# Kernel optimization log

Measured on AMD Instinct MI355X. Metric: run time of the kernel, lower is better.

The kernel has to match this reference:

```python
import jax, jax.numpy as jnp
import numpy as np

N_NODES = 100000
N_EDGES = 3200000
D_IN = 128
D_OUT = 128


def setup_inputs() -> dict:
    key = jax.random.key(0)
    ks = jax.random.split(key, 7)
    x = jax.random.normal(ks[0], (N_NODES, D_IN), dtype=jnp.float32)
    weight = jax.random.normal(ks[1], (D_IN, D_OUT), dtype=jnp.float32) * (1.0 / np.sqrt(D_OUT))
    bias = jax.random.normal(ks[2], (D_OUT,), dtype=jnp.float32) * (1.0 / np.sqrt(D_OUT))
    adj_rows = jax.random.randint(ks[3], (N_EDGES,), 0, N_NODES, dtype=jnp.int32)
    adj_cols = jax.random.randint(ks[4], (N_EDGES,), 0, N_NODES, dtype=jnp.int32)
    adj_vals = jax.random.uniform(ks[5], (N_EDGES,), dtype=jnp.float32)
    # norm kept in [0.5, 1.5) to avoid division blow-up (degree-like normalizer)
    norm = jax.random.uniform(ks[6], (N_NODES, 1), dtype=jnp.float32) + 0.5
    return {"x": x, "weight": weight, "bias": bias,
            "adj_rows": adj_rows, "adj_cols": adj_cols, "adj_vals": adj_vals,
            "norm": norm}


def reference(x, weight, bias, adj_rows, adj_cols, adj_vals, norm):
    # support = input @ W               [N, D_OUT]
    support = x @ weight
    # output = spmm(adj, support): gather source rows, scale by edge value,
    # scatter-add into destination rows.
    gathered = support[adj_cols] * adj_vals[:, None]          # [E, D_OUT]
    output = jax.ops.segment_sum(gathered, adj_rows, num_segments=x.shape[0])
    output = output / norm
    return output + bias
```

## Files before the change

kernel.cpp:

```cpp
#include <hip/hip_runtime.h>

#define M_NODES 100000
#define N_EDGES 3200000
#define D 128
#define NBUCK 1563
#define GEMM_BLOCKS 1563
#define HIST_CHUNK 12288
#define HIST_BLOCKS 261
#define FILL_CHUNK 6144
#define FILL_BLOCKS 521
#define BUCK_CAP 4096

#define OFF_SUP16  0ull
#define OFF_BCNT   25600000ull
#define OFF_BSTART 25606400ull
#define OFF_BPOS   25612800ull
#define OFF_REC    25619200ull
#define WS_NEEDED  51219200ull

__device__ __forceinline__ unsigned short f2bf(float f) {
    unsigned u = __float_as_uint(f);
    u += 0x7fff + ((u >> 16) & 1);
    return (unsigned short)(u >> 16);
}
__device__ __forceinline__ float2 bfpair(unsigned u) {
    float2 r;
    r.x = __uint_as_float(u << 16);
    r.y = __uint_as_float(u & 0xffff0000u);
    return r;
}

__global__ __launch_bounds__(256) void gemm_hist_kernel(const float* __restrict__ x,
                                                        const float* __restrict__ w,
                                                        unsigned* __restrict__ sup16,
                                                        const int* __restrict__ rows,
                                                        int* __restrict__ bcnt,
                                                        int M) {
    __shared__ __align__(16) char smem[24576];
    const int tid = threadIdx.x;

    if (blockIdx.x >= GEMM_BLOCKS) {
        int* h = (int*)smem;
        const int hb = blockIdx.x - GEMM_BLOCKS;
        for (int i = tid; i < NBUCK; i += 256) h[i] = 0;
        __syncthreads();
        const long long base = (long long)hb * HIST_CHUNK;
#pragma unroll
        for (int i = 0; i < 12; ++i) {
            const long long e = base + (i * 256 + tid) * 4;
            if (e < N_EDGES) {
                const int4 r = *(const int4*)&rows[e];
                atomicAdd(&h[r.x >> 6], 1);
                atomicAdd(&h[r.y >> 6], 1);
                atomicAdd(&h[r.z >> 6], 1);
                atomicAdd(&h[r.w >> 6], 1);
            }
        }
        __syncthreads();
        for (int i = tid; i < NBUCK; i += 256)
            if (h[i]) atomicAdd(&bcnt[i], h[i]);
        return;
    }

    float (*sX)[64]  = (float(*)[64])smem;
    float (*sW)[128] = (float(*)[128])(smem + 8192);

    const int r0 = blockIdx.x * 64;
    const int tx = tid & 31;
    const int ty = tid >> 5;

    float acc[8][4];
#pragma unroll
    for (int r = 0; r < 8; ++r)
#pragma unroll
        for (int c = 0; c < 4; ++c) acc[r][c] = 0.f;

    for (int c0 = 0; c0 < 128; c0 += 32) {
        {
            const int row = tid >> 3;
            const int kk  = (tid & 7) * 4;
#pragma unroll
            for (int h = 0; h < 2; ++h) {
                const int rr = row + h * 32;
                float4 v = make_float4(0.f, 0.f, 0.f, 0.f);
                if (r0 + rr < M)
                    v = *(const float4*)&x[(size_t)(r0 + rr) * D + c0 + kk];
                sX[kk + 0][rr] = v.x;
                sX[kk + 1][rr] = v.y;
                sX[kk + 2][rr] = v.z;
                sX[kk + 3][rr] = v.w;
            }
        }
#pragma unroll
        for (int i = tid; i < 1024; i += 256) {
            const int k  = i >> 5;
            const int c4 = (i & 31) * 4;
            *(float4*)&sW[k][c4] = *(const float4*)&w[(size_t)(c0 + k) * D + c4];
        }
        __syncthreads();

#pragma unroll
        for (int k = 0; k < 32; ++k) {
            const float4 wv = *(const float4*)&sW[k][tx * 4];
            const float4 xa = *(const float4*)&sX[k][ty * 8];
            const float4 xb = *(const float4*)&sX[k][ty * 8 + 4];
            const float xr[8] = {xa.x, xa.y, xa.z, xa.w, xb.x, xb.y, xb.z, xb.w};
#pragma unroll
            for (int r = 0; r < 8; ++r) {
                acc[r][0] += xr[r] * wv.x;
                acc[r][1] += xr[r] * wv.y;
                acc[r][2] += xr[r] * wv.z;
                acc[r][3] += xr[r] * wv.w;
            }
        }
        __syncthreads();
    }

#pragma unroll
    for (int r = 0; r < 8; ++r) {
        const int row = r0 + ty * 8 + r;
        if (row < M) {
            uint2 p;
            p.x = (unsigned)f2bf(acc[r][0]) | ((unsigned)f2bf(acc[r][1]) << 16);
            p.y = (unsigned)f2bf(acc[r][2]) | ((unsigned)f2bf(acc[r][3]) << 16);
            *(uint2*)&sup16[(size_t)row * 64 + tx * 2] = p;
        }
    }
}

__global__ __launch_bounds__(256) void scan_kernel(const int* __restrict__ bcnt,
                                                   int* __restrict__ bstart,
                                                   int* __restrict__ bpos) {
    __shared__ int tsum[256];
    const int t = threadIdx.x;
    int local[7];
    int s = 0;
#pragma unroll
    for (int k = 0; k < 7; ++k) {
        const int idx = t * 7 + k;
        const int v = (idx < NBUCK) ? bcnt[idx] : 0;
        local[k] = v;
        s += v;
    }
    tsum[t] = s;
    __syncthreads();
    for (int off = 1; off < 256; off <<= 1) {
        const int v = (t >= off) ? tsum[t - off] : 0;
        __syncthreads();
        tsum[t] += v;
        __syncthreads();
    }
    int pos = tsum[t] - s;
#pragma unroll
    for (int k = 0; k < 7; ++k) {
        const int idx = t * 7 + k;
        if (idx < NBUCK) {
            bstart[idx] = pos;
            bpos[idx]   = pos;
            pos += local[k];
        }
    }
    if (t == 0) bstart[NBUCK] = N_EDGES;
}

__global__ __launch_bounds__(256) void fill_kernel(const int* __restrict__ rows,
                                                   const int* __restrict__ cols,
                                                   const float* __restrict__ vals,
                                                   int* __restrict__ bpos,
                                                   int2* __restrict__ rec) {
    __shared__ int cnt[NBUCK];
    __shared__ int bas[NBUCK];
    __shared__ unsigned short lrank[FILL_CHUNK];
    const int t = threadIdx.x;
    for (int i = t; i < NBUCK; i += 256) cnt[i] = 0;
    __syncthreads();
    const long long base = (long long)blockIdx.x * FILL_CHUNK;

#pragma unroll
    for (int i = 0; i < 6; ++i) {
        const int li = (i * 256 + t) * 4;
        const long long e = base + li;
        if (e < N_EDGES) {
            const int4 r = *(const int4*)&rows[e];
            lrank[li + 0] = (unsigned short)atomicAdd(&cnt[r.x >> 6], 1);
            lrank[li + 1] = (unsigned short)atomicAdd(&cnt[r.y >> 6], 1);
            lrank[li + 2] = (unsigned short)atomicAdd(&cnt[r.z >> 6], 1);
            lrank[li + 3] = (unsigned short)atomicAdd(&cnt[r.w >> 6], 1);
        }
    }
    __syncthreads();
    for (int i = t; i < NBUCK; i += 256)
        bas[i] = cnt[i] ? atomicAdd(&bpos[i], cnt[i]) : 0;
    __syncthreads();
#pragma unroll
    for (int i = 0; i < 6; ++i) {
        const int li = (i * 256 + t) * 4;
        const long long e = base + li;
        if (e < N_EDGES) {
            const int4   r = *(const int4*)&rows[e];
            const int4   c = *(const int4*)&cols[e];
            const float4 v = *(const float4*)&vals[e];
            int p;
            p = bas[r.x >> 6] + lrank[li + 0];
            rec[p] = make_int2(c.x | ((r.x & 63) << 20), __float_as_int(v.x));
            p = bas[r.y >> 6] + lrank[li + 1];
            rec[p] = make_int2(c.y | ((r.y & 63) << 20), __float_as_int(v.y));
            p = bas[r.z >> 6] + lrank[li + 2];
            rec[p] = make_int2(c.z | ((r.z & 63) << 20), __float_as_int(v.z));
            p = bas[r.w >> 6] + lrank[li + 3];
            rec[p] = make_int2(c.w | ((r.w & 63) << 20), __float_as_int(v.w));
        }
    }
}

__global__ __launch_bounds__(512) void gather_kernel(const unsigned* __restrict__ sup16,
                                                     const int* __restrict__ bstart,
                                                     const int2* __restrict__ rec,
                                                     const float* __restrict__ norm,
                                                     const float* __restrict__ bias,
                                                     float* __restrict__ out) {
    __shared__ int2 elist[BUCK_CAP];
    __shared__ unsigned short lrank[BUCK_CAP];
    __shared__ int cnt[64];
    __shared__ int rbase[65];
    const int tid = threadIdx.x;
    const int b   = blockIdx.x;

    if (tid < 64) cnt[tid] = 0;
    __syncthreads();
    const int s0 = bstart[b];
    const int n  = min(bstart[b + 1] - s0, BUCK_CAP);

    for (int k = tid; k < n; k += 512) {
        const int rl = (rec[s0 + k].x >> 20) & 63;
        lrank[k] = (unsigned short)atomicAdd(&cnt[rl], 1);
    }
    __syncthreads();
    if (tid == 0) {
        int run = 0;
#pragma unroll
        for (int i = 0; i < 64; ++i) {
            rbase[i] = run;
            run += cnt[i];
        }
        rbase[64] = run;
    }
    __syncthreads();
    for (int k = tid; k < n; k += 512) {
        const int2 e = rec[s0 + k];
        elist[rbase[(e.x >> 20) & 63] + lrank[k]] = make_int2(e.x & 0xFFFFF, e.y);
    }
    __syncthreads();

    const int w    = tid >> 6;
    const int lane = tid & 63;
    const unsigned* __restrict__ supl = sup16 + lane;
    const int fo = lane * 2;
    const float2 b2 = *(const float2*)&bias[fo];

#pragma unroll 1
    for (int rr = 0; rr < 8; ++rr) {
        const int rl  = w * 8 + rr;
        const int row = b * 64 + rl;
        if (row >= M_NODES) break;
        const int j0 = rbase[rl];
        const int j1 = rbase[rl + 1];
        float2 acc = make_float2(0.f, 0.f);
        int j = j0;
        for (; j + 8 <= j1; j += 8) {
            int2 e[8];
#pragma unroll
            for (int q = 0; q < 8; ++q) e[q] = elist[j + q];
            unsigned u[8];
#pragma unroll
            for (int q = 0; q < 8; ++q) u[q] = supl[(unsigned)e[q].x << 6];
#pragma unroll
            for (int q = 0; q < 8; ++q) {
                const float v = __int_as_float(e[q].y);
                const float2 p = bfpair(u[q]);
                acc.x = fmaf(p.x, v, acc.x);
                acc.y = fmaf(p.y, v, acc.y);
            }
        }
        for (; j + 2 <= j1; j += 2) {
            const int2 e0 = elist[j];
            const int2 e1 = elist[j + 1];
            const unsigned u0 = supl[(unsigned)e0.x << 6];
            const unsigned u1 = supl[(unsigned)e1.x << 6];
            const float2 p0 = bfpair(u0);
            const float2 p1 = bfpair(u1);
            const float v0 = __int_as_float(e0.y);
            const float v1 = __int_as_float(e1.y);
            acc.x = fmaf(p0.x, v0, acc.x);
            acc.y = fmaf(p0.y, v0, acc.y);
            acc.x = fmaf(p1.x, v1, acc.x);
            acc.y = fmaf(p1.y, v1, acc.y);
        }
        for (; j < j1; ++j) {
            const int2 e = elist[j];
            const unsigned u = supl[(unsigned)e.x << 6];
            const float v = __int_as_float(e.y);
            const float2 p = bfpair(u);
            acc.x = fmaf(p.x, v, acc.x);
            acc.y = fmaf(p.y, v, acc.y);
        }
        const float inv = 1.0f / norm[row];
        float2 o;
        o.x = fmaf(acc.x, inv, b2.x);
        o.y = fmaf(acc.y, inv, b2.y);
        *(float2*)&out[(size_t)row * D + fo] = o;
    }
}

__global__ __launch_bounds__(256) void gemm32_kernel(const float* __restrict__ x,
                                                     const float* __restrict__ w,
                                                     float* __restrict__ support,
                                                     int M) {
    __shared__ float sX[32][64];
    __shared__ float sW[32][128];
    const int tid = threadIdx.x;
    const int r0  = blockIdx.x * 64;
    const int tx  = tid & 31;
    const int ty  = tid >> 5;
    float acc[8][4];
#pragma unroll
    for (int r = 0; r < 8; ++r)
#pragma unroll
        for (int c = 0; c < 4; ++c) acc[r][c] = 0.f;
    for (int c0 = 0; c0 < 128; c0 += 32) {
        {
            const int row = tid >> 3;
            const int kk  = (tid & 7) * 4;
#pragma unroll
            for (int h = 0; h < 2; ++h) {
                const int rr = row + h * 32;
                float4 v = make_float4(0.f, 0.f, 0.f, 0.f);
                if (r0 + rr < M)
                    v = *(const float4*)&x[(size_t)(r0 + rr) * D + c0 + kk];
                sX[kk + 0][rr] = v.x; sX[kk + 1][rr] = v.y;
                sX[kk + 2][rr] = v.z; sX[kk + 3][rr] = v.w;
            }
        }
#pragma unroll
        for (int i = tid; i < 1024; i += 256) {
            const int k  = i >> 5;
            const int c4 = (i & 31) * 4;
            *(float4*)&sW[k][c4] = *(const float4*)&w[(size_t)(c0 + k) * D + c4];
        }
        __syncthreads();
#pragma unroll
        for (int k = 0; k < 32; ++k) {
            const float4 wv = *(const float4*)&sW[k][tx * 4];
            const float4 xa = *(const float4*)&sX[k][ty * 8];
            const float4 xb = *(const float4*)&sX[k][ty * 8 + 4];
            const float xr[8] = {xa.x, xa.y, xa.z, xa.w, xb.x, xb.y, xb.z, xb.w};
#pragma unroll
            for (int r = 0; r < 8; ++r) {
                acc[r][0] += xr[r] * wv.x; acc[r][1] += xr[r] * wv.y;
                acc[r][2] += xr[r] * wv.z; acc[r][3] += xr[r] * wv.w;
            }
        }
        __syncthreads();
    }
#pragma unroll
    for (int r = 0; r < 8; ++r) {
        const int row = r0 + ty * 8 + r;
        if (row < M)
            *(float4*)&support[(size_t)row * D + tx * 4] =
                make_float4(acc[r][0], acc[r][1], acc[r][2], acc[r][3]);
    }
}

__global__ __launch_bounds__(256) void spmm_kernel(const float* __restrict__ support,
                                                   const int* __restrict__ rows,
                                                   const int* __restrict__ cols,
                                                   const float* __restrict__ vals,
                                                   float* __restrict__ out) {
    const long long t = (long long)blockIdx.x * 256 + threadIdx.x;
    const int e = (int)(t >> 5);
    if (e >= N_EDGES) return;
    const int f   = (int)(t & 31) * 4;
    const int src = cols[e];
    const int dst = rows[e];
    const float v = vals[e];
    const float4 s = *(const float4*)&support[(size_t)src * D + f];
    float* o = &out[(size_t)dst * D + f];
    atomicAdd(o + 0, s.x * v);
    atomicAdd(o + 1, s.y * v);
    atomicAdd(o + 2, s.z * v);
    atomicAdd(o + 3, s.w * v);
}

__global__ __launch_bounds__(256) void finalize_kernel(float* __restrict__ out,
                                                       const float* __restrict__ norm,
                                                       const float* __restrict__ bias) {
    const int t = blockIdx.x * 256 + threadIdx.x;
    const int nrow = t >> 5;
    if (nrow >= M_NODES) return;
    const int f = (t & 31) * 4;
    const float inv = 1.0f / norm[nrow];
    float4 o = *(float4*)&out[(size_t)nrow * D + f];
    const float4 b = *(const float4*)&bias[f];
    o.x = o.x * inv + b.x; o.y = o.y * inv + b.y;
    o.z = o.z * inv + b.z; o.w = o.w * inv + b.w;
    *(float4*)&out[(size_t)nrow * D + f] = o;
}

extern "C" void kernel_launch(void* const* d_in, const int* in_sizes, int n_in,
                              void* d_out, int out_size, void* d_ws, size_t ws_size,
                              hipStream_t stream) {
    const float* x    = (const float*)d_in[0];
    const float* w    = (const float*)d_in[1];
    const float* bias = (const float*)d_in[2];
    const int*   rows = (const int*)d_in[3];
    const int*   cols = (const int*)d_in[4];
    const float* vals = (const float*)d_in[5];
    const float* norm = (const float*)d_in[6];
    float* out = (float*)d_out;
    char* ws = (char*)d_ws;

    if (ws_size >= WS_NEEDED) {
        unsigned* sup16  = (unsigned*)(ws + OFF_SUP16);
        int*      bcnt   = (int*)(ws + OFF_BCNT);
        int*      bstart = (int*)(ws + OFF_BSTART);
        int*      bpos   = (int*)(ws + OFF_BPOS);
        int2*     rec    = (int2*)(ws + OFF_REC);

        hipMemsetAsync(bcnt, 0, NBUCK * sizeof(int), stream);
        gemm_hist_kernel<<<GEMM_BLOCKS + HIST_BLOCKS, 256, 0, stream>>>(x, w, sup16,
                                                                        rows, bcnt, M_NODES);
        scan_kernel<<<1, 256, 0, stream>>>(bcnt, bstart, bpos);
        fill_kernel<<<FILL_BLOCKS, 256, 0, stream>>>(rows, cols, vals, bpos, rec);
        gather_kernel<<<NBUCK, 512, 0, stream>>>(sup16, bstart, rec,
                                                 norm, bias, out);
    } else {
        float* support = (float*)ws;
        gemm32_kernel<<<(M_NODES + 63) / 64, 256, 0, stream>>>(x, w, support, M_NODES);
        hipMemsetAsync(d_out, 0, (size_t)out_size * sizeof(float), stream);
        const long long spmm_threads = (long long)N_EDGES * 32;
        spmm_kernel<<<(int)((spmm_threads + 255) / 256), 256, 0, stream>>>(support, rows, cols, vals, out);
        finalize_kernel<<<(M_NODES * 32 + 255) / 256, 256, 0, stream>>>(out, norm, bias);
    }
}
```

Measured before the change: 370.7 us.

## Use fixed-capacity bucket slots to drop histogram pass and scan kernel

Replaces the histogram, prefix-scan, and fill pipeline with a single fill pass that writes edge records into fixed-capacity per-bucket slots (BUCK_CAP each), with offsets claimed by a global atomicAdd on the bucket counter. The fill is fused into the GEMM launch, which removes one full read of rows and two kernel launches. The gather kernel now does its per-row reordering with shared-memory atomics instead of a separate rank array. In exchange the workspace grows to hold padded buckets, and any bucket with more than BUCK_CAP edges silently drops records.

```diff
diff --git a/kernel.cpp b/kernel.cpp
--- a/kernel.cpp
+++ b/kernel.cpp
@@ -5,18 +5,15 @@
 #define D 128
 #define NBUCK 1563
 #define GEMM_BLOCKS 1563
-#define HIST_CHUNK 12288
-#define HIST_BLOCKS 261
 #define FILL_CHUNK 6144
 #define FILL_BLOCKS 521
+#define PREP_BLOCKS (FILL_BLOCKS + GEMM_BLOCKS)
 #define BUCK_CAP 4096
 
 #define OFF_SUP16  0ull
 #define OFF_BCNT   25600000ull
-#define OFF_BSTART 25606400ull
-#define OFF_BPOS   25612800ull
-#define OFF_REC    25619200ull
-#define WS_NEEDED  51219200ull
+#define OFF_REC    25608192ull
+#define WS_NEEDED  76824576ull
 
 __device__ __forceinline__ unsigned short f2bf(float f) {
     unsigned u = __float_as_uint(f);
@@ -30,42 +27,76 @@
     return r;
 }
 
-__global__ __launch_bounds__(256) void gemm_hist_kernel(const float* __restrict__ x,
-                                                        const float* __restrict__ w,
-                                                        unsigned* __restrict__ sup16,
-                                                        const int* __restrict__ rows,
-                                                        int* __restrict__ bcnt,
-                                                        int M) {
-    __shared__ __align__(16) char smem[24576];
+__global__ __launch_bounds__(256) void prep_kernel(const float* __restrict__ x,
+                                                   const float* __restrict__ w,
+                                                   unsigned* __restrict__ sup16,
+                                                   const int* __restrict__ rows,
+                                                   const int* __restrict__ cols,
+                                                   const float* __restrict__ vals,
+                                                   int* __restrict__ bcnt,
+                                                   int2* __restrict__ rec,
+                                                   int M) {
+    __shared__ __align__(16) char smem[25088];
     const int tid = threadIdx.x;
 
-    if (blockIdx.x >= GEMM_BLOCKS) {
-        int* h = (int*)smem;
-        const int hb = blockIdx.x - GEMM_BLOCKS;
-        for (int i = tid; i < NBUCK; i += 256) h[i] = 0;
-        __syncthreads();
-        const long long base = (long long)hb * HIST_CHUNK;
-#pragma unroll
-        for (int i = 0; i < 12; ++i) {
-            const long long e = base + (i * 256 + tid) * 4;
+    if (blockIdx.x < FILL_BLOCKS) {
+        int* cnt = (int*)smem;
+        int* bas = (int*)(smem + 6256);
+        unsigned short* lrank = (unsigned short*)(smem + 12512);
+        for (int i = tid; i < NBUCK; i += 256) cnt[i] = 0;
+        __syncthreads();
+        const long long base = (long long)blockIdx.x * FILL_CHUNK;
+
+#pragma unroll
+        for (int i = 0; i < 6; ++i) {
+            const int li = (i * 256 + tid) * 4;
+            const long long e = base + li;
             if (e < N_EDGES) {
                 const int4 r = *(const int4*)&rows[e];
-                atomicAdd(&h[r.x >> 6], 1);
-                atomicAdd(&h[r.y >> 6], 1);
-                atomicAdd(&h[r.z >> 6], 1);
-                atomicAdd(&h[r.w >> 6], 1);
+                lrank[li + 0] = (unsigned short)atomicAdd(&cnt[r.x >> 6], 1);
+                lrank[li + 1] = (unsigned short)atomicAdd(&cnt[r.y >> 6], 1);
+                lrank[li + 2] = (unsigned short)atomicAdd(&cnt[r.z >> 6], 1);
+                lrank[li + 3] = (unsigned short)atomicAdd(&cnt[r.w >> 6], 1);
             }
         }
         __syncthreads();
         for (int i = tid; i < NBUCK; i += 256)
-            if (h[i]) atomicAdd(&bcnt[i], h[i]);
+            bas[i] = cnt[i] ? atomicAdd(&bcnt[i], cnt[i]) : 0;
+        __syncthreads();
+#pragma unroll
+        for (int i = 0; i < 6; ++i) {
+            const int li = (i * 256 + tid) * 4;
+            const long long e = base + li;
+            if (e < N_EDGES) {
+                const int4   r = *(const int4*)&rows[e];
+                const int4   c = *(const int4*)&cols[e];
+                const float4 v = *(const float4*)&vals[e];
+                int p;
+                p = bas[r.x >> 6] + lrank[li + 0];
+                if (p < BUCK_CAP)
+                    rec[(size_t)(r.x >> 6) * BUCK_CAP + p] =
+                        make_int2(c.x | ((r.x & 63) << 20), __float_as_int(v.x));
+                p = bas[r.y >> 6] + lrank[li + 1];
+                if (p < BUCK_CAP)
+                    rec[(size_t)(r.y >> 6) * BUCK_CAP + p] =
+                        make_int2(c.y | ((r.y & 63) << 20), __float_as_int(v.y));
+                p = bas[r.z >> 6] + lrank[li + 2];
+                if (p < BUCK_CAP)
+                    rec[(size_t)(r.z >> 6) * BUCK_CAP + p] =
+                        make_int2(c.z | ((r.z & 63) << 20), __float_as_int(v.z));
+                p = bas[r.w >> 6] + lrank[li + 3];
+                if (p < BUCK_CAP)
+                    rec[(size_t)(r.w >> 6) * BUCK_CAP + p] =
+                        make_int2(c.w | ((r.w & 63) << 20), __float_as_int(v.w));
+            }
+        }
         return;
     }
 
     float (*sX)[64]  = (float(*)[64])smem;
     float (*sW)[128] = (float(*)[128])(smem + 8192);
 
-    const int r0 = blockIdx.x * 64;
+    const int r0 = (blockIdx.x - FILL_BLOCKS) * 64;
     const int tx = tid & 31;
     const int ty = tid >> 5;
 
@@ -128,99 +159,13 @@
     }
 }
 
-__global__ __launch_bounds__(256) void scan_kernel(const int* __restrict__ bcnt,
-                                                   int* __restrict__ bstart,
-                                                   int* __restrict__ bpos) {
-    __shared__ int tsum[256];
-    const int t = threadIdx.x;
-    int local[7];
-    int s = 0;
-#pragma unroll
-    for (int k = 0; k < 7; ++k) {
-        const int idx = t * 7 + k;
-        const int v = (idx < NBUCK) ? bcnt[idx] : 0;
-        local[k] = v;
-        s += v;
-    }
-    tsum[t] = s;
-    __syncthreads();
-    for (int off = 1; off < 256; off <<= 1) {
-        const int v = (t >= off) ? tsum[t - off] : 0;
-        __syncthreads();
-        tsum[t] += v;
-        __syncthreads();
-    }
-    int pos = tsum[t] - s;
-#pragma unroll
-    for (int k = 0; k < 7; ++k) {
-        const int idx = t * 7 + k;
-        if (idx < NBUCK) {
-            bstart[idx] = pos;
-            bpos[idx]   = pos;
-            pos += local[k];
-        }
-    }
-    if (t == 0) bstart[NBUCK] = N_EDGES;
-}
-
-__global__ __launch_bounds__(256) void fill_kernel(const int* __restrict__ rows,
-                                                   const int* __restrict__ cols,
-                                                   const float* __restrict__ vals,
-                                                   int* __restrict__ bpos,
-                                                   int2* __restrict__ rec) {
-    __shared__ int cnt[NBUCK];
-    __shared__ int bas[NBUCK];
-    __shared__ unsigned short lrank[FILL_CHUNK];
-    const int t = threadIdx.x;
-    for (int i = t; i < NBUCK; i += 256) cnt[i] = 0;
-    __syncthreads();
-    const long long base = (long long)blockIdx.x * FILL_CHUNK;
-
-#pragma unroll
-    for (int i = 0; i < 6; ++i) {
-        const int li = (i * 256 + t) * 4;
-        const long long e = base + li;
-        if (e < N_EDGES) {
-            const int4 r = *(const int4*)&rows[e];
-            lrank[li + 0] = (unsigned short)atomicAdd(&cnt[r.x >> 6], 1);
-            lrank[li + 1] = (unsigned short)atomicAdd(&cnt[r.y >> 6], 1);
-            lrank[li + 2] = (unsigned short)atomicAdd(&cnt[r.z >> 6], 1);
-            lrank[li + 3] = (unsigned short)atomicAdd(&cnt[r.w >> 6], 1);
-        }
-    }
-    __syncthreads();
-    for (int i = t; i < NBUCK; i += 256)
-        bas[i] = cnt[i] ? atomicAdd(&bpos[i], cnt[i]) : 0;
-    __syncthreads();
-#pragma unroll
-    for (int i = 0; i < 6; ++i) {
-        const int li = (i * 256 + t) * 4;
-        const long long e = base + li;
-        if (e < N_EDGES) {
-            const int4   r = *(const int4*)&rows[e];
-            const int4   c = *(const int4*)&cols[e];
-            const float4 v = *(const float4*)&vals[e];
-            int p;
-            p = bas[r.x >> 6] + lrank[li + 0];
-            rec[p] = make_int2(c.x | ((r.x & 63) << 20), __float_as_int(v.x));
-            p = bas[r.y >> 6] + lrank[li + 1];
-            rec[p] = make_int2(c.y | ((r.y & 63) << 20), __float_as_int(v.y));
-            p = bas[r.z >> 6] + lrank[li + 2];
-            rec[p] = make_int2(c.z | ((r.z & 63) << 20), __float_as_int(v.z));
-            p = bas[r.w >> 6] + lrank[li + 3];
-            rec[p] = make_int2(c.w | ((r.w & 63) << 20), __float_as_int(v.w));
-        }
-    }
-}
-
 __global__ __launch_bounds__(512) void gather_kernel(const unsigned* __restrict__ sup16,
-                                                     const int* __restrict__ bstart,
+                                                     const int* __restrict__ bcnt,
                                                      const int2* __restrict__ rec,
                                                      const float* __restrict__ norm,
                                                      const float* __restrict__ bias,
                                                      float* __restrict__ out) {
     __shared__ int2 elist[BUCK_CAP];
-    __shared__ unsigned short lrank[BUCK_CAP];
     __shared__ int cnt[64];
     __shared__ int rbase[65];
     const int tid = threadIdx.x;
@@ -228,13 +173,11 @@
 
     if (tid < 64) cnt[tid] = 0;
     __syncthreads();
-    const int s0 = bstart[b];
-    const int n  = min(bstart[b + 1] - s0, BUCK_CAP);
-
-    for (int k = tid; k < n; k += 512) {
-        const int rl = (rec[s0 + k].x >> 20) & 63;
-        lrank[k] = (unsigned short)atomicAdd(&cnt[rl], 1);
-    }
+    const int n = min(bcnt[b], BUCK_CAP);
+    const int2* __restrict__ recb = rec + (size_t)b * BUCK_CAP;
+
+    for (int k = tid; k < n; k += 512)
+        atomicAdd(&cnt[(recb[k].x >> 20) & 63], 1);
     __syncthreads();
     if (tid == 0) {
         int run = 0;
@@ -246,9 +189,12 @@
         rbase[64] = run;
     }
     __syncthreads();
+    if (tid < 64) cnt[tid] = rbase[tid];
+    __syncthreads();
     for (int k = tid; k < n; k += 512) {
-        const int2 e = rec[s0 + k];
-        elist[rbase[(e.x >> 20) & 63] + lrank[k]] = make_int2(e.x & 0xFFFFF, e.y);
+        const int2 e = recb[k];
+        const int p = atomicAdd(&cnt[(e.x >> 20) & 63], 1);
+        elist[p] = make_int2(e.x & 0xFFFFF, e.y);
     }
     __syncthreads();
 
@@ -420,18 +366,14 @@
     char* ws = (char*)d_ws;
 
     if (ws_size >= WS_NEEDED) {
-        unsigned* sup16  = (unsigned*)(ws + OFF_SUP16);
-        int*      bcnt   = (int*)(ws + OFF_BCNT);
-        int*      bstart = (int*)(ws + OFF_BSTART);
-        int*      bpos   = (int*)(ws + OFF_BPOS);
-        int2*     rec    = (int2*)(ws + OFF_REC);
+        unsigned* sup16 = (unsigned*)(ws + OFF_SUP16);
+        int*      bcnt  = (int*)(ws + OFF_BCNT);
+        int2*     rec   = (int2*)(ws + OFF_REC);
 
         hipMemsetAsync(bcnt, 0, NBUCK * sizeof(int), stream);
-        gemm_hist_kernel<<<GEMM_BLOCKS + HIST_BLOCKS, 256, 0, stream>>>(x, w, sup16,
-                                                                        rows, bcnt, M_NODES);
-        scan_kernel<<<1, 256, 0, stream>>>(bcnt, bstart, bpos);
-        fill_kernel<<<FILL_BLOCKS, 256, 0, stream>>>(rows, cols, vals, bpos, rec);
-        gather_kernel<<<NBUCK, 512, 0, stream>>>(sup16, bstart, rec,
+        prep_kernel<<<PREP_BLOCKS, 256, 0, stream>>>(x, w, sup16, rows, cols, vals,
+                                                     bcnt, rec, M_NODES);
+        gather_kernel<<<NBUCK, 512, 0, stream>>>(sup16, bcnt, rec,
                                                  norm, bias, out);
     } else {
         float* support = (float*)ws;
```

Result: faster. 342.5 us (-7.6%).
